# Optimization experiments

Measured on AMD Instinct MI355X. Metric: run time of the kernel, lower is better.

The kernel has to match this reference:

```python
import jax, jax.numpy as jnp
import numpy as np


def setup_inputs() -> dict:
    key = jax.random.key(0)
    k1, k2 = jax.random.split(key)
    B, T, V = 128, 256, 256
    batch = jax.random.normal(k1, (B, T, V, 3), dtype=jnp.float32)
    missing = jax.random.uniform(k2, (B, T, V)) < 0.2
    labels = jnp.where(missing, -1.0, 1.0)
    batch = batch.at[..., 0].set(labels)
    return {"batch": batch}


def reference(batch):
    B, T, V, _ = batch.shape
    dt = batch.dtype
    # constant-velocity model matrices (hardcoded in the module)
    F = jnp.array([[1, 0, 1, 0], [0, 1, 0, 1], [0, 0, 1, 0], [0, 0, 0, 1]], dtype=dt)
    H = jnp.array([[1, 0, 0, 0], [0, 1, 0, 0]], dtype=dt)
    Q = jnp.eye(4, dtype=dt) * 0.01
    R = jnp.eye(2, dtype=dt) * 1.0
    I4 = jnp.eye(4, dtype=dt)

    s0 = jnp.zeros((B, V, 4), dtype=dt)
    P0 = jnp.broadcast_to(jnp.eye(4, dtype=dt) * 1000.0, (B, V, 4, 4))

    obs_t = jnp.moveaxis(batch, 1, 0)  # (T, B, V, 3)

    def step(carry, obs):
        s, P = carry  # s: (B,V,4), P: (B,V,4,4)
        labels = obs[..., 0]
        z = obs[..., 1:]                       # (B,V,2)
        mask = (labels != -1)[..., None]       # (B,V,1)
        s_pred = jnp.einsum('bvj,ij->bvi', s, F)                 # s @ F.T
        P_pred = jnp.einsum('ij,bvjk,lk->bvil', F, P, F) + Q     # F P F^T + Q
        y = (z - s_pred[..., :2]) * mask                          # (B,V,2)
        S = P_pred[..., :2, :2] + R                               # H P H^T + R
        K = jnp.einsum('bvij,bvjk->bvik', P_pred[..., :, :2], jnp.linalg.inv(S))  # (B,V,4,2)
        s_upd = s_pred + jnp.einsum('bvij,bvj->bvi', K, y) * mask
        KH = jnp.einsum('bvij,jk->bvik', K, H)                    # (B,V,4,4)
        P_upd = jnp.einsum('bvij,bvjk->bvik', I4 - KH, P_pred)
        s_new = jnp.where(mask, s_upd, s_pred)
        P_new = jnp.where(mask[..., None], P_upd, P_pred)
        return (s_new, P_new), None

    (s_final, _), _ = jax.lax.scan(step, (s0, P0), obs_t)
    last_pos = s_final[..., :2]                                   # (B,V,2)
    ones = jnp.ones((B, V, 1), dtype=dt)
    return jnp.concatenate((ones, last_pos), axis=-1)             # (B,V,3)
```

## Files before the change

kernel.cpp:

```cpp
#include <hip/hip_runtime.h>


#define KF_B 128
#define KF_T 256
#define KF_V 256
#define KF_G 32

__global__ __launch_bounds__(64) void kf_kernel(const float* __restrict__ batch,
                                                float* __restrict__ out) {
    const int tid = blockIdx.x * 64 + threadIdx.x;
    const int b = tid >> 8;
    const int v = tid & (KF_V - 1);

    const float* __restrict__ ptr = batch + ((size_t)b * KF_T * KF_V + v) * 3;
    const int stride = KF_V * 3;

    float p00 = 1000.f, p01 = 0.f, p11 = 1000.f;
    float x0 = 0.f, v0 = 0.f;
    float x1 = 0.f, v1 = 0.f;

    float bufA[KF_G][3], bufB[KF_G][3];

#define KF_LOAD(dst)                               \
    do {                                           \
        _Pragma("unroll")                          \
        for (int k = 0; k < KF_G; ++k) {           \
            (dst)[k][0] = ptr[k * stride + 0];     \
            (dst)[k][1] = ptr[k * stride + 1];     \
            (dst)[k][2] = ptr[k * stride + 2];     \
        }                                          \
        ptr += KF_G * stride;                      \
    } while (0)

#define KF_STEP(obs)                                                    \
    do {                                                                \
        const float label = (obs)[0];                                   \
        const float z0 = (obs)[1];                                      \
        const float z1 = (obs)[2];                                      \
                                                           \
        const float xp0 = x0 + v0;                                      \
        const float xp1 = x1 + v1;                                      \
        const float q00 = p00 + 2.f * p01 + p11 + 0.01f;                \
        const float q01 = p01 + p11;                                    \
        const float q11 = p11 + 0.01f;                                  \
                    \
        const float S = q00 + 1.f;                                      \
        const float m = (label != -1.0f) ? 1.0f : 0.0f;                 \
        const float is = m * __builtin_amdgcn_rcpf(S);                  \
        const float K0 = q00 * is;                                      \
        const float K1 = q01 * is;                                      \
                                   \
        const float y0 = z0 - xp0;                                      \
        const float y1 = z1 - xp1;                                      \
        x0 = xp0 + K0 * y0;                                             \
        v0 = v0 + K1 * y0;                                              \
        x1 = xp1 + K0 * y1;                                             \
        v1 = v1 + K1 * y1;                                              \
                                                 \
        p00 = q00 - K0 * q00;                                           \
        p01 = q01 - K0 * q01;                                           \
        p11 = q11 - K1 * q01;                                           \
    } while (0)

    KF_LOAD(bufA);

    const int NG = KF_T / KF_G;
    for (int g = 0; g < NG; g += 2) {
        KF_LOAD(bufB);
#pragma unroll
        for (int k = 0; k < KF_G; ++k) KF_STEP(bufA[k]);
        if (g + 2 < NG) {
            KF_LOAD(bufA);
        }
#pragma unroll
        for (int k = 0; k < KF_G; ++k) KF_STEP(bufB[k]);
    }

    float* o = out + (size_t)tid * 3;
    o[0] = 1.0f;
    o[1] = x0;
    o[2] = x1;
}

extern "C" void kernel_launch(void* const* d_in, const int* in_sizes, int n_in,
                              void* d_out, int out_size, void* d_ws, size_t ws_size,
                              hipStream_t stream) {
    (void)in_sizes; (void)n_in; (void)d_ws; (void)ws_size; (void)out_size;
    const float* batch = (const float*)d_in[0];
    float* out = (float*)d_out;
    const int total = KF_B * KF_V;
    kf_kernel<<<total / 64, 64, 0, stream>>>(batch, out);
}
```

Measured before the change: 147.5 us.

## Load timesteps with inline-asm dwordx4 global loads and explicit vmcnt pipelining

Replaces the per-scalar strided loads with inline-assembly global_load_dwordx4 instructions that use SGPR bases and immediate offsets. Each 16-byte load covers one timestep's three floats plus one spare, and the last load of each group is shifted back by 4 bytes so it stays in bounds. Four groups of four steps are issued, and each is waited on with a graded s_waitcnt vmcnt, so loads overlap with compute while register use drops. The approach relies on hand-written vmcnt accounting and over-fetches a third more bytes than it uses, and launch_bounds now asks for 1 block per CU.

```diff
diff --git a/kernel.cpp b/kernel.cpp
--- a/kernel.cpp
+++ b/kernel.cpp
@@ -1,57 +1,48 @@
 #include <hip/hip_runtime.h>
+#include <stdint.h>
 
 
 #define KF_B 128
 #define KF_T 256
 #define KF_V 256
-#define KF_G 32
 
-__global__ __launch_bounds__(64) void kf_kernel(const float* __restrict__ batch,
-                                                float* __restrict__ out) {
-    const int tid = blockIdx.x * 64 + threadIdx.x;
-    const int b = tid >> 8;
-    const int v = tid & (KF_V - 1);
+typedef float f4 __attribute__((ext_vector_type(4)));
 
-    const float* __restrict__ ptr = batch + ((size_t)b * KF_T * KF_V + v) * 3;
-    const int stride = KF_V * 3;
+#define GLOAD(dst, sbase, imm)                                         \
+    asm volatile("global_load_dwordx4 %0, %1, %2 offset:" #imm         \
+                 : "=v"(dst) : "v"(voff), "s"(sbase) : "memory")
 
-    float p00 = 1000.f, p01 = 0.f, p11 = 1000.f;
-    float x0 = 0.f, v0 = 0.f;
-    float x1 = 0.f, v1 = 0.f;
+#define WAITVM(N, B)                                                   \
+    asm volatile("s_waitcnt vmcnt(" #N ")"                             \
+                 : "+v"((B)[0]), "+v"((B)[1]),                         \
+                   "+v"((B)[2]), "+v"((B)[3]) :: "memory")
 
-    float bufA[KF_G][3], bufB[KF_G][3];
-
-#define KF_LOAD(dst)                               \
-    do {                                           \
-        _Pragma("unroll")                          \
-        for (int k = 0; k < KF_G; ++k) {           \
-            (dst)[k][0] = ptr[k * stride + 0];     \
-            (dst)[k][1] = ptr[k * stride + 1];     \
-            (dst)[k][2] = ptr[k * stride + 2];     \
-        }                                          \
-        ptr += KF_G * stride;                      \
+#define KF_ISSUE(buf)                          \
+    do {                                       \
+        GLOAD((buf)[0], sb0, 0);               \
+        GLOAD((buf)[1], sb0, 3072);            \
+        GLOAD((buf)[2], sb1, 0);               \
+        GLOAD((buf)[3], sb1, 3068);            \
+        sb0 += 12288; sb1 += 12288;            \
     } while (0)
 
-#define KF_STEP(obs)                                                    \
+#define KF_STEP3(label, z0, z1)                                         \
     do {                                                                \
-        const float label = (obs)[0];                                   \
-        const float z0 = (obs)[1];                                      \
-        const float z1 = (obs)[2];                                      \
                                                            \
         const float xp0 = x0 + v0;                                      \
         const float xp1 = x1 + v1;                                      \
         const float q00 = p00 + 2.f * p01 + p11 + 0.01f;                \
         const float q01 = p01 + p11;                                    \
         const float q11 = p11 + 0.01f;                                  \
-                    \
+                       \
         const float S = q00 + 1.f;                                      \
-        const float m = (label != -1.0f) ? 1.0f : 0.0f;                 \
+        const float m = ((label) != -1.0f) ? 1.0f : 0.0f;               \
         const float is = m * __builtin_amdgcn_rcpf(S);                  \
         const float K0 = q00 * is;                                      \
         const float K1 = q01 * is;                                      \
                                    \
-        const float y0 = z0 - xp0;                                      \
-        const float y1 = z1 - xp1;                                      \
+        const float y0 = (z0) - xp0;                                    \
+        const float y1 = (z1) - xp1;                                    \
         x0 = xp0 + K0 * y0;                                             \
         v0 = v0 + K1 * y0;                                              \
         x1 = xp1 + K0 * y1;                                             \
@@ -62,20 +53,42 @@
         p11 = q11 - K1 * q01;                                           \
     } while (0)
 
-    KF_LOAD(bufA);
+#define KF_CONSUME(B)                                        \
+    do {                                                     \
+        KF_STEP3((B)[0][0], (B)[0][1], (B)[0][2]);           \
+        KF_STEP3((B)[1][0], (B)[1][1], (B)[1][2]);           \
+        KF_STEP3((B)[2][0], (B)[2][1], (B)[2][2]);           \
+        KF_STEP3((B)[3][1], (B)[3][2], (B)[3][3]);           \
+    } while (0)
 
-    const int NG = KF_T / KF_G;
-    for (int g = 0; g < NG; g += 2) {
-        KF_LOAD(bufB);
-#pragma unroll
-        for (int k = 0; k < KF_G; ++k) KF_STEP(bufA[k]);
-        if (g + 2 < NG) {
-            KF_LOAD(bufA);
-        }
-#pragma unroll
-        for (int k = 0; k < KF_G; ++k) KF_STEP(bufB[k]);
+__global__ __launch_bounds__(64, 1) void kf_kernel(const float* __restrict__ batch,
+                                                   float* __restrict__ out) {
+    const int blk = blockIdx.x;
+    const int b = blk >> 2;
+    const int v = ((blk & 3) << 6) | threadIdx.x;
+
+    const uint32_t voff = (uint32_t)v * 12u;
+    uint64_t sb0 = (uint64_t)batch + (uint64_t)b * (KF_T * KF_V * 3 * 4);
+    uint64_t sb1 = sb0 + 6144;
+
+    float p00 = 1000.f, p01 = 0.f, p11 = 1000.f;
+    float x0 = 0.f, v0 = 0.f;
+    float x1 = 0.f, v1 = 0.f;
+
+#pragma unroll 1
+    for (int body = 0; body < 16; ++body) {
+        f4 g0[4], g1[4], g2[4], g3[4];
+        KF_ISSUE(g0);
+        KF_ISSUE(g1);
+        KF_ISSUE(g2);
+        KF_ISSUE(g3);
+        WAITVM(12, g0); KF_CONSUME(g0);
+        WAITVM(8,  g1); KF_CONSUME(g1);
+        WAITVM(4,  g2); KF_CONSUME(g2);
+        WAITVM(0,  g3); KF_CONSUME(g3);
     }
 
+    const int tid = blk * 64 + threadIdx.x;
     float* o = out + (size_t)tid * 3;
     o[0] = 1.0f;
     o[1] = x0;
```

Result: no change. 144.9 us (-1.7%).

## Split time scan into chunks with affine-map composition across chunks

Applied to the files above, without the earlier changes.

The serial 256-step scan per track is split into 8 time chunks, each processed by a separate block. The covariance recursion does not depend on the data, only on the labels, so each chunk first replays the label-only P recursion up to its start, then accumulates the affine state map for its 32 steps into workspace. A second kernel composes the 8 maps per track to produce the final position. This multiplies thread-level parallelism (the base grid has only 512 blocks of 64 threads) at the cost of redundant label reads and P updates for the warm-up prefix, plus a second launch and a workspace round trip.

```diff
diff --git a/kernel.cpp b/kernel.cpp
--- a/kernel.cpp
+++ b/kernel.cpp
@@ -1,82 +1,97 @@
 #include <hip/hip_runtime.h>
+#include <stdint.h>
 
 
 #define KF_B 128
 #define KF_T 256
 #define KF_V 256
-#define KF_G 32
+#define KF_C 8
+#define KF_L 32
+#define KF_NT (KF_B * KF_V)
 
-__global__ __launch_bounds__(64) void kf_kernel(const float* __restrict__ batch,
-                                                float* __restrict__ out) {
-    const int tid = blockIdx.x * 64 + threadIdx.x;
-    const int b = tid >> 8;
-    const int v = tid & (KF_V - 1);
+#define KF_PK(label)                                                    \
+    const float q00 = p00 + 2.f * p01 + p11 + 0.01f;                    \
+    const float q01 = p01 + p11;                                        \
+    const float q11 = p11 + 0.01f;                                      \
+    const float S = q00 + 1.f;                                          \
+    const float m = ((label) != -1.0f) ? 1.0f : 0.0f;                   \
+    const float is = m * __builtin_amdgcn_rcpf(S);                      \
+    const float K0 = q00 * is;                                          \
+    const float K1 = q01 * is;                                          \
+    p00 = q00 - K0 * q00;                                               \
+    p01 = q01 - K0 * q01;                                               \
+    p11 = q11 - K1 * q01;
 
-    const float* __restrict__ ptr = batch + ((size_t)b * KF_T * KF_V + v) * 3;
+__global__ __launch_bounds__(64) void kf_scan(const float* __restrict__ batch,
+                                              float* __restrict__ ws) {
+    const int blk = blockIdx.x;
+    const int chunk = blk & (KF_C - 1);
+    const int trackblk = blk >> 3;
+    const int track = trackblk * 64 + threadIdx.x;
+    const int b = track >> 8;
+    const int v = track & (KF_V - 1);
+
+    const float* __restrict__ base =
+        batch + ((size_t)b * KF_T * KF_V + v) * 3;
     const int stride = KF_V * 3;
 
     float p00 = 1000.f, p01 = 0.f, p11 = 1000.f;
-    float x0 = 0.f, v0 = 0.f;
-    float x1 = 0.f, v1 = 0.f;
 
-    float bufA[KF_G][3], bufB[KF_G][3];
-
-#define KF_LOAD(dst)                               \
-    do {                                           \
-        _Pragma("unroll")                          \
-        for (int k = 0; k < KF_G; ++k) {           \
-            (dst)[k][0] = ptr[k * stride + 0];     \
-            (dst)[k][1] = ptr[k * stride + 1];     \
-            (dst)[k][2] = ptr[k * stride + 2];     \
-        }                                          \
-        ptr += KF_G * stride;                      \
-    } while (0)
-
-#define KF_STEP(obs)                                                    \
-    do {                                                                \
-        const float label = (obs)[0];                                   \
-        const float z0 = (obs)[1];                                      \
-        const float z1 = (obs)[2];                                      \
-                                                           \
-        const float xp0 = x0 + v0;                                      \
-        const float xp1 = x1 + v1;                                      \
-        const float q00 = p00 + 2.f * p01 + p11 + 0.01f;                \
-        const float q01 = p01 + p11;                                    \
-        const float q11 = p11 + 0.01f;                                  \
-                    \
-        const float S = q00 + 1.f;                                      \
-        const float m = (label != -1.0f) ? 1.0f : 0.0f;                 \
-        const float is = m * __builtin_amdgcn_rcpf(S);                  \
-        const float K0 = q00 * is;                                      \
-        const float K1 = q01 * is;                                      \
-                                   \
-        const float y0 = z0 - xp0;                                      \
-        const float y1 = z1 - xp1;                                      \
-        x0 = xp0 + K0 * y0;                                             \
-        v0 = v0 + K1 * y0;                                              \
-        x1 = xp1 + K0 * y1;                                             \
-        v1 = v1 + K1 * y1;                                              \
-                                                 \
-        p00 = q00 - K0 * q00;                                           \
-        p01 = q01 - K0 * q01;                                           \
-        p11 = q11 - K1 * q01;                                           \
-    } while (0)
-
-    KF_LOAD(bufA);
-
-    const int NG = KF_T / KF_G;
-    for (int g = 0; g < NG; g += 2) {
-        KF_LOAD(bufB);
-#pragma unroll
-        for (int k = 0; k < KF_G; ++k) KF_STEP(bufA[k]);
-        if (g + 2 < NG) {
-            KF_LOAD(bufA);
-        }
-#pragma unroll
-        for (int k = 0; k < KF_G; ++k) KF_STEP(bufB[k]);
+    const int warmT = KF_L * chunk;
+    const float* p = base;
+    for (int t = 0; t < warmT; ++t) {
+        const float label = p[0];
+        p += stride;
+        KF_PK(label);
     }
 
-    float* o = out + (size_t)tid * 3;
+    float m00 = 1.f, m01 = 0.f, m10 = 0.f, m11 = 1.f;
+    float d0p = 0.f, d0v = 0.f, d1p = 0.f, d1v = 0.f;
+
+    for (int t = 0; t < KF_L; ++t) {
+        const float label = p[0];
+        const float z0 = p[1];
+        const float z1 = p[2];
+        p += stride;
+        KF_PK(label);
+        const float a = 1.f - K0;
+        const float t00 = m00 + m10;
+        const float t01 = m01 + m11;
+        m00 = a * t00;
+        m01 = a * t01;
+        m10 = m10 - K1 * t00;
+        m11 = m11 - K1 * t01;
+        const float s0 = d0p + d0v;
+        d0p = a * s0 + K0 * z0;
+        d0v = d0v + K1 * (z0 - s0);
+        const float s1 = d1p + d1v;
+        d1p = a * s1 + K0 * z1;
+        d1v = d1v + K1 * (z1 - s1);
+    }
+
+    float* w = ws + ((size_t)chunk * KF_NT + track) * 8;
+    float4 w0 = make_float4(m00, m01, m10, m11);
+    float4 w1 = make_float4(d0p, d0v, d1p, d1v);
+    *(float4*)(w) = w0;
+    *(float4*)(w + 4) = w1;
+}
+
+__global__ __launch_bounds__(64) void kf_compose(const float* __restrict__ ws,
+                                                 float* __restrict__ out) {
+    const int track = blockIdx.x * 64 + threadIdx.x;
+    float x0 = 0.f, v0 = 0.f, x1 = 0.f, v1 = 0.f;
+#pragma unroll
+    for (int c = 0; c < KF_C; ++c) {
+        const float* w = ws + ((size_t)c * KF_NT + track) * 8;
+        const float4 a = *(const float4*)(w);
+        const float4 d = *(const float4*)(w + 4);
+        const float nx0 = a.x * x0 + a.y * v0 + d.x;
+        const float nv0 = a.z * x0 + a.w * v0 + d.y;
+        const float nx1 = a.x * x1 + a.y * v1 + d.z;
+        const float nv1 = a.z * x1 + a.w * v1 + d.w;
+        x0 = nx0; v0 = nv0; x1 = nx1; v1 = nv1;
+    }
+    float* o = out + (size_t)track * 3;
     o[0] = 1.0f;
     o[1] = x0;
     o[2] = x1;
@@ -85,9 +100,11 @@
 extern "C" void kernel_launch(void* const* d_in, const int* in_sizes, int n_in,
                               void* d_out, int out_size, void* d_ws, size_t ws_size,
                               hipStream_t stream) {
-    (void)in_sizes; (void)n_in; (void)d_ws; (void)ws_size; (void)out_size;
+    (void)in_sizes; (void)n_in; (void)ws_size; (void)out_size;
     const float* batch = (const float*)d_in[0];
     float* out = (float*)d_out;
-    const int total = KF_B * KF_V;
-    kf_kernel<<<total / 64, 64, 0, stream>>>(batch, out);
+    float* ws = (float*)d_ws;
+
+    kf_scan<<<KF_C * KF_NT / 64, 64, 0, stream>>>(batch, ws);
+    kf_compose<<<KF_NT / 64, 64, 0, stream>>>(ws, out);
 }
```

After: 228.9 us. +55.3%, slower.
